# Kernel optimization log

Measured on AMD Instinct MI355X. Metric: run time of the kernel, lower is better.

## Reference

```python
import jax, jax.numpy as jnp
import numpy as np

NUM_HEADS = 16


def setup_inputs() -> dict:
    key = jax.random.key(0)
    ks = jax.random.split(key, 5)
    b, s, d = 2, 2048, 1024
    std = (2.0 / (d + d)) ** 0.5
    x = jax.random.normal(ks[0], (b, s, d), dtype=jnp.float32)
    Wq = jax.random.normal(ks[1], (d, d), dtype=jnp.float32) * std
    Wk = jax.random.normal(ks[2], (d, d), dtype=jnp.float32) * std
    Wv = jax.random.normal(ks[3], (d, d), dtype=jnp.float32) * std
    Wo = jax.random.normal(ks[4], (d, d), dtype=jnp.float32) * std
    return {"x": x, "Wq": Wq, "Wk": Wk, "Wv": Wv, "Wo": Wo}


def reference(x, Wq, Wk, Wv, Wo):
    b, s, d = x.shape
    h = NUM_HEADS
    dk = d // h
    # projections: bias-free x @ W (W is [in, out])
    def split_heads(t):
        return t.reshape(b, s, h, dk).transpose(0, 2, 1, 3)  # b h s dk
    q = split_heads(x @ Wq)
    k = split_heads(x @ Wk)
    v = split_heads(x @ Wv)
    scale = 1.0 / jnp.sqrt(jnp.asarray(dk, dtype=x.dtype))
    scores = jnp.einsum('bhqd,bhkd->bhqk', q, k) * scale  # b h s s
    causal = jnp.tril(jnp.ones((s, s), dtype=bool))
    scores = jnp.where(causal, scores, -jnp.inf)
    probs = jax.nn.softmax(scores, axis=-1)
    out = jnp.einsum('bhqk,bhkd->bhqd', probs, v)
    out = out.transpose(0, 2, 1, 3).reshape(b, s, d)  # b s (h dk)
    return out @ Wo
```

## Files before the change

kernel.cpp:

```cpp
#include <hip/hip_runtime.h>

typedef unsigned short u16;
typedef unsigned int   u32;

using bf16x8 = __attribute__((ext_vector_type(8))) __bf16;
using bf16x4 = __attribute__((ext_vector_type(4))) __bf16;
using f32x4  = __attribute__((ext_vector_type(4))) float;
using s16x4  = __attribute__((ext_vector_type(4))) short;

#define NH    16
#define DKH   64
#define SEQ   2048
#define BAT   2
#define DMOD  1024

#define QSCALE 0.18033688011112042f

__device__ __forceinline__ u16 f2bf(float f) {
  union { float f; u32 u; } v; v.f = f;
  u32 r = v.u + 0x7fffu + ((v.u >> 16) & 1u);
  return (u16)(r >> 16);
}

__device__ __forceinline__ u32 pack2bf(float a, float b) {
  union { float f; u32 u; } x, y; x.f = a; y.f = b;
  u32 ua = x.u + 0x7fffu + ((x.u >> 16) & 1u);
  u32 ub = y.u + 0x7fffu + ((y.u >> 16) & 1u);
  return __builtin_amdgcn_perm(ub, ua, 0x07060302u);
}

__device__ __forceinline__ s16x4 pk4bf(float a, float b, float c, float d) {
  union { bf16x4 bv; s16x4 sv; } u;
  u.bv[0] = (__bf16)a; u.bv[1] = (__bf16)b; u.bv[2] = (__bf16)c; u.bv[3] = (__bf16)d;
  return u.sv;
}

#if __has_builtin(__builtin_amdgcn_exp2f)
#define EXP2(x) __builtin_amdgcn_exp2f(x)
#else
#define EXP2(x) exp2f(x)
#endif

#if __has_builtin(__builtin_amdgcn_mfma_f32_16x16x16bf16_1k)
__device__ __forceinline__ f32x4 mfma16(s16x4 a, s16x4 b, f32x4 c) {
  return __builtin_amdgcn_mfma_f32_16x16x16bf16_1k(a, b, c, 0, 0, 0);
}
#else
__device__ __forceinline__ f32x4 mfma16(s16x4 a, s16x4 b, f32x4 c) {
  f32x4 d;
  asm volatile("v_mfma_f32_16x16x16_bf16 %0, %1, %2, %3\n\ts_nop 7\n\ts_nop 7"
               : "=v"(d) : "v"(a), "v"(b), "v"(c));
  return d;
}
#endif

typedef const __attribute__((address_space(1))) u32 glb_u32;
typedef __attribute__((address_space(3))) u32 lds_u32;
__device__ __forceinline__ void gload16(const u16* g, u16* l) {
  __builtin_amdgcn_global_load_lds((glb_u32*)(const void*)g, (lds_u32*)(void*)l, 16, 0, 0);
}

__global__ __launch_bounds__(256) void transpose_all(const float* __restrict__ Wq,
                                                     const float* __restrict__ Wk,
                                                     const float* __restrict__ Wv,
                                                     const float* __restrict__ Wo,
                                                     u16* __restrict__ Wt) {
  __shared__ u16 t[32][33];
  const float* W = blockIdx.z == 0 ? Wq : blockIdx.z == 1 ? Wk : blockIdx.z == 2 ? Wv : Wo;
  u16* o = Wt + (size_t)blockIdx.z * DMOD * DMOD;
  int bx = blockIdx.x * 32, by = blockIdx.y * 32;
  int x = threadIdx.x, y = threadIdx.y;
  #pragma unroll
  for (int i = 0; i < 32; i += 8)
    t[y + i][x] = f2bf(W[(size_t)(by + y + i) * DMOD + bx + x]);
  __syncthreads();
  #pragma unroll
  for (int i = 0; i < 32; i += 8)
    o[(size_t)(bx + y + i) * DMOD + by + x] = t[x][y + i];
}

__global__ __launch_bounds__(256) void convert_x(const float* __restrict__ x,
                                                 u16* __restrict__ xb) {
  size_t i = ((size_t)blockIdx.x * 256 + threadIdx.x) * 8;
  float4 f0 = *(const float4*)(x + i);
  float4 f1 = *(const float4*)(x + i + 4);
  uint4 o;
  o.x = pack2bf(f0.x, f0.y); o.y = pack2bf(f0.z, f0.w);
  o.z = pack2bf(f1.x, f1.y); o.w = pack2bf(f1.z, f1.w);
  *(uint4*)(xb + i) = o;
}

__global__ __launch_bounds__(256, 3) void gemm_qkv(const u16* __restrict__ A,
                                                   const u16* __restrict__ Bt,
                                                   u16* __restrict__ Qo,
                                                   u16* __restrict__ Ko,
                                                   u16* __restrict__ Vo) {
  __shared__ __align__(16) u16 As[128 * 32];
  __shared__ __align__(16) u16 Bs[128 * 32];
  const int tid  = threadIdx.x;
  const int lane = tid & 63, wv = tid >> 6;
  const int wm   = wv >> 1, wn = wv & 1;
  const int lrow = lane & 15, quad = lane >> 4;
  const int tileM = blockIdx.x * 128, tileN = blockIdx.y * 128;

  const f32x4 fz = {0.f, 0.f, 0.f, 0.f};
  f32x4 acc[4][4];
  #pragma unroll
  for (int i = 0; i < 4; ++i)
    #pragma unroll
    for (int j = 0; j < 4; ++j) acc[i][j] = fz;

  for (int kt = 0; kt < DMOD; kt += 32) {
    if (kt) __syncthreads();
    #pragma unroll
    for (int i = 0; i < 2; ++i) {
      int idx = i * 256 + tid;
      gload16(&A [(size_t)(tileM + (idx >> 2)) * DMOD + kt + (idx & 3) * 8], &As[idx * 8]);
      gload16(&Bt[(size_t)(tileN + (idx >> 2)) * DMOD + kt + (idx & 3) * 8], &Bs[idx * 8]);
    }
    __syncthreads();

    bf16x8 af[4], bfr[4];
    #pragma unroll
    for (int mt = 0; mt < 4; ++mt)
      af[mt] = *(const bf16x8*)(&As[(wm * 64 + mt * 16 + lrow) * 32 + quad * 8]);
    #pragma unroll
    for (int nt = 0; nt < 4; ++nt)
      bfr[nt] = *(const bf16x8*)(&Bs[(wn * 64 + nt * 16 + lrow) * 32 + quad * 8]);
    #pragma unroll
    for (int mt = 0; mt < 4; ++mt)
      #pragma unroll
      for (int nt = 0; nt < 4; ++nt)
        acc[mt][nt] = __builtin_amdgcn_mfma_f32_16x16x32_bf16(af[mt], bfr[nt],
                                                              acc[mt][nt], 0, 0, 0);
  }

  #pragma unroll
  for (int mt = 0; mt < 4; ++mt) {
    #pragma unroll
    for (int nt = 0; nt < 4; ++nt) {
      int gm0 = tileM + wm * 64 + mt * 16 + quad * 4;
      int gn  = tileN + wn * 64 + nt * 16 + lrow;
      int which = gn >> 10, col = gn & 1023;
      int bb = gm0 >> 11, srw0 = gm0 & (SEQ - 1);
      int hh = col >> 6, dki = col & (DKH - 1);
      size_t bhi = (size_t)(bb * NH + hh);
      if (which == 0) {
        #pragma unroll
        for (int r = 0; r < 4; ++r)
          Qo[(bhi * SEQ + srw0 + r) * DKH + dki] = f2bf(acc[mt][nt][r] * QSCALE);
      } else if (which == 1) {
        #pragma unroll
        for (int r = 0; r < 4; ++r)
          Ko[(bhi * SEQ + srw0 + r) * DKH + dki] = f2bf(acc[mt][nt][r]);
      } else {
        uint2 pk;
        pk.x = pack2bf(acc[mt][nt][0], acc[mt][nt][1]);
        pk.y = pack2bf(acc[mt][nt][2], acc[mt][nt][3]);
        *(uint2*)(&Vo[(((bhi * (SEQ / 4)) + (srw0 >> 2)) * DKH + dki) * 4]) = pk;
      }
    }
  }
}

__global__ __launch_bounds__(256, 3) void gemm_out(const u16* __restrict__ A,
                                                   const u16* __restrict__ Bt,
                                                   float* __restrict__ Co) {
  __shared__ __align__(16) u16 As[128 * 32];
  __shared__ __align__(16) u16 Bs[64 * 32];
  const int tid  = threadIdx.x;
  const int lane = tid & 63, wv = tid >> 6;
  const int wm   = wv & 1, wn = wv >> 1;
  const int lrow = lane & 15, quad = lane >> 4;
  const int tileM = blockIdx.x * 128, tileN = blockIdx.y * 64;

  const f32x4 fz = {0.f, 0.f, 0.f, 0.f};
  f32x4 acc[4][2];
  #pragma unroll
  for (int i = 0; i < 4; ++i) { acc[i][0] = fz; acc[i][1] = fz; }

  for (int kt = 0; kt < DMOD; kt += 32) {
    if (kt) __syncthreads();
    #pragma unroll
    for (int i = 0; i < 2; ++i) {
      int idx = i * 256 + tid;
      gload16(&A[(size_t)(tileM + (idx >> 2)) * DMOD + kt + (idx & 3) * 8], &As[idx * 8]);
    }
    gload16(&Bt[(size_t)(tileN + (tid >> 2)) * DMOD + kt + (tid & 3) * 8], &Bs[tid * 8]);
    __syncthreads();

    bf16x8 af[4], bfr[2];
    #pragma unroll
    for (int mt = 0; mt < 4; ++mt)
      af[mt] = *(const bf16x8*)(&As[(wm * 64 + mt * 16 + lrow) * 32 + quad * 8]);
    #pragma unroll
    for (int nt = 0; nt < 2; ++nt)
      bfr[nt] = *(const bf16x8*)(&Bs[(wn * 32 + nt * 16 + lrow) * 32 + quad * 8]);
    #pragma unroll
    for (int mt = 0; mt < 4; ++mt)
      #pragma unroll
      for (int nt = 0; nt < 2; ++nt)
        acc[mt][nt] = __builtin_amdgcn_mfma_f32_16x16x32_bf16(af[mt], bfr[nt],
                                                              acc[mt][nt], 0, 0, 0);
  }

  #pragma unroll
  for (int mt = 0; mt < 4; ++mt)
    #pragma unroll
    for (int nt = 0; nt < 2; ++nt)
      #pragma unroll
      for (int r = 0; r < 4; ++r) {
        int gm = tileM + wm * 64 + mt * 16 + quad * 4 + r;
        int gn = tileN + wn * 32 + nt * 16 + lrow;
        Co[(size_t)gm * DMOD + gn] = acc[mt][nt][r];
      }
}

#define KP 72
#define VP 132
#define OP 68

__global__ __launch_bounds__(256, 2) void attn_k(const u16* __restrict__ Q,
                                                 const u16* __restrict__ Kg,
                                                 const u16* __restrict__ Vg,
                                                 u16* __restrict__ Og) {
  __shared__ __align__(16) u16 KsA[128 * KP];
  __shared__ __align__(16) u16 VsA[64 * VP];
  __shared__ __align__(16) u16 KsB[128 * KP];
  __shared__ __align__(16) u16 VsB[64 * VP];

  const int tid  = threadIdx.x;
  const int lane = tid & 63, w = tid >> 6;
  const int lrow = lane & 15, quad = lane >> 4;
  const int bh = blockIdx.x;
  const int t  = blockIdx.y;
  const int qt = (t < 8) ? t : 23 - t;
  const int b = bh >> 4, h = bh & 15;

  const u16* Qbh = Q  + (size_t)bh * SEQ * DKH;
  const u16* Kbh = Kg + (size_t)bh * SEQ * DKH;
  const u16* Vbh = Vg + (size_t)bh * SEQ * DKH;

  const int jmax = qt;

  bf16x8 bq[2][2];
  #pragma unroll
  for (int s = 0; s < 2; ++s)
    #pragma unroll
    for (int kk = 0; kk < 2; ++kk)
      bq[s][kk] = *(const bf16x8*)(&Qbh[(size_t)(qt * 128 + (2 * w + s) * 16 + lrow) * DKH
                                        + kk * 32 + quad * 8]);

  uint4 kreg[4], vreg[4];
  #pragma unroll
  for (int k = 0; k < 4; ++k) {
    int ci = k * 256 + tid;
    kreg[k] = *(const uint4*)(&Kbh[(size_t)(ci >> 3) * DKH + (ci & 7) * 8]);
    vreg[k] = *(const uint4*)(&Vbh[(size_t)(ci >> 5) * 256 + (ci & 31) * 8]);
  }

  const f32x4 fz = {0.f, 0.f, 0.f, 0.f};
  f32x4 oacc[2][4];
  #pragma unroll
  for (int s = 0; s < 2; ++s)
    #pragma unroll
    for (int d = 0; d < 4; ++d) oacc[s][d] = fz;
  float lsum[2] = {0.f, 0.f};

  int cur = 0;
  for (int j = 0; j <= jmax; ++j) {
    u16* Ks = cur ? KsB : KsA;
    u16* Vs = cur ? VsB : VsA;

    #pragma unroll
    for (int k = 0; k < 4; ++k) {
      int ci = k * 256 + tid;
      *(uint4*)(&Ks[(ci >> 3) * KP + (ci & 7) * 8]) = kreg[k];
      int sq = ci >> 5, dkp = ci & 31;
      union { uint4 q; uint2 d[2]; } vv; vv.q = vreg[k];
      *(uint2*)(&Vs[(2 * dkp)     * VP + 4 * sq]) = vv.d[0];
      *(uint2*)(&Vs[(2 * dkp + 1) * VP + 4 * sq]) = vv.d[1];
    }

    if (j < jmax) {
      const int jn = j + 1;
      #pragma unroll
      for (int k = 0; k < 4; ++k) {
        int ci = k * 256 + tid;
        kreg[k] = *(const uint4*)(&Kbh[(size_t)(jn * 128 + (ci >> 3)) * DKH + (ci & 7) * 8]);
        vreg[k] = *(const uint4*)(&Vbh[(size_t)(jn * 32 + (ci >> 5)) * 256 + (ci & 31) * 8]);
      }
    }

    __syncthreads();

    if (j < jmax) {
      __builtin_amdgcn_s_setprio(1);
      f32x4 sacc[2][8];
      #pragma unroll
      for (int s = 0; s < 2; ++s)
        #pragma unroll
        for (int m = 0; m < 8; ++m) sacc[s][m] = fz;
      #pragma unroll
      for (int kk = 0; kk < 2; ++kk)
        #pragma unroll
        for (int m = 0; m < 8; ++m) {
          bf16x8 ak = *(const bf16x8*)(&Ks[(m * 16 + lrow) * KP + kk * 32 + quad * 8]);
          sacc[0][m] = __builtin_amdgcn_mfma_f32_16x16x32_bf16(ak, bq[0][kk], sacc[0][m], 0, 0, 0);
          sacc[1][m] = __builtin_amdgcn_mfma_f32_16x16x32_bf16(ak, bq[1][kk], sacc[1][m], 0, 0, 0);
        }
      #pragma unroll
      for (int m = 0; m < 8; ++m) {
        float p00 = EXP2(sacc[0][m][0]), p01 = EXP2(sacc[0][m][1]);
        float p02 = EXP2(sacc[0][m][2]), p03 = EXP2(sacc[0][m][3]);
        float p10 = EXP2(sacc[1][m][0]), p11 = EXP2(sacc[1][m][1]);
        float p12 = EXP2(sacc[1][m][2]), p13 = EXP2(sacc[1][m][3]);
        lsum[0] += (p00 + p01) + (p02 + p03);
        lsum[1] += (p10 + p11) + (p12 + p13);
        s16x4 pk0 = pk4bf(p00, p01, p02, p03);
        s16x4 pk1 = pk4bf(p10, p11, p12, p13);
        #pragma unroll
        for (int d = 0; d < 4; ++d) {
          s16x4 av = *(const s16x4*)(&Vs[(d * 16 + lrow) * VP + m * 16 + quad * 4]);
          oacc[0][d] = mfma16(av, pk0, oacc[0][d]);
          oacc[1][d] = mfma16(av, pk1, oacc[1][d]);
        }
      }
      __builtin_amdgcn_s_setprio(0);
    } else {
      #pragma unroll
      for (int s = 0; s < 2; ++s) {
        const int ss = 2 * w + s;
        for (int m = 0; m < ss; ++m) {
          f32x4 sv = fz;
          #pragma unroll
          for (int kk = 0; kk < 2; ++kk) {
            bf16x8 ak = *(const bf16x8*)(&Ks[(m * 16 + lrow) * KP + kk * 32 + quad * 8]);
            sv = __builtin_amdgcn_mfma_f32_16x16x32_bf16(ak, bq[s][kk], sv, 0, 0, 0);
          }
          float p0 = EXP2(sv[0]), p1 = EXP2(sv[1]), p2 = EXP2(sv[2]), p3 = EXP2(sv[3]);
          lsum[s] += (p0 + p1) + (p2 + p3);
          s16x4 pk = pk4bf(p0, p1, p2, p3);
          #pragma unroll
          for (int d = 0; d < 4; ++d) {
            s16x4 av = *(const s16x4*)(&Vs[(d * 16 + lrow) * VP + m * 16 + quad * 4]);
            oacc[s][d] = mfma16(av, pk, oacc[s][d]);
          }
        }
        {
          f32x4 sv = fz;
          #pragma unroll
          for (int kk = 0; kk < 2; ++kk) {
            bf16x8 ak = *(const bf16x8*)(&Ks[(ss * 16 + lrow) * KP + kk * 32 + quad * 8]);
            sv = __builtin_amdgcn_mfma_f32_16x16x32_bf16(ak, bq[s][kk], sv, 0, 0, 0);
          }
          float p[4];
          #pragma unroll
          for (int r = 0; r < 4; ++r)
            p[r] = (quad * 4 + r > lrow) ? 0.f : EXP2(sv[r]);
          lsum[s] += (p[0] + p[1]) + (p[2] + p[3]);
          s16x4 pk = pk4bf(p[0], p[1], p[2], p[3]);
          #pragma unroll
          for (int d = 0; d < 4; ++d) {
            s16x4 av = *(const s16x4*)(&Vs[(d * 16 + lrow) * VP + ss * 16 + quad * 4]);
            oacc[s][d] = mfma16(av, pk, oacc[s][d]);
          }
        }
      }
    }
    cur ^= 1;
  }

  float inv[2];
  #pragma unroll
  for (int s = 0; s < 2; ++s) {
    float v = lsum[s];
    v += __shfl_xor(v, 16, 64);
    v += __shfl_xor(v, 32, 64);
    inv[s] = 1.f / v;
  }

  __syncthreads();
  u16* Osr = KsA;
  #pragma unroll
  for (int s = 0; s < 2; ++s) {
    int row = (2 * w + s) * 16 + lrow;
    #pragma unroll
    for (int d = 0; d < 4; ++d) {
      uint2 pkk;
      pkk.x = pack2bf(oacc[s][d][0] * inv[s], oacc[s][d][1] * inv[s]);
      pkk.y = pack2bf(oacc[s][d][2] * inv[s], oacc[s][d][3] * inv[s]);
      *(uint2*)(&Osr[row * OP + d * 16 + quad * 4]) = pkk;
    }
  }
  __syncthreads();
  #pragma unroll
  for (int k = 0; k < 4; ++k) {
    int c = k * 256 + tid;
    int row = c >> 3, ch = c & 7;
    uint4 v = *(const uint4*)(&Osr[row * OP + ch * 8]);
    *(uint4*)(&Og[(size_t)(b * SEQ + qt * 128 + row) * DMOD + h * DKH + ch * 8]) = v;
  }
}

extern "C" void kernel_launch(void* const* d_in, const int* in_sizes, int n_in,
                              void* d_out, int out_size, void* d_ws, size_t ws_size,
                              hipStream_t stream) {
  const float* x  = (const float*)d_in[0];
  const float* Wq = (const float*)d_in[1];
  const float* Wk = (const float*)d_in[2];
  const float* Wv = (const float*)d_in[3];
  const float* Wo = (const float*)d_in[4];

  u16* ws = (u16*)d_ws;
  const size_t WSZ = (size_t)DMOD * DMOD;
  const size_t TSZ = (size_t)BAT * NH * SEQ * DKH;
  u16* Wt  = ws;
  u16* Wto = Wt + 3 * WSZ;
  u16* xb  = Wt + 4 * WSZ;
  u16* Qb  = xb + TSZ;
  u16* Kb  = Qb + TSZ;
  u16* Vb  = Kb + TSZ;
  u16* Ob  = xb;

  transpose_all<<<dim3(32, 32, 4), dim3(32, 8), 0, stream>>>(Wq, Wk, Wv, Wo, Wt);
  convert_x<<<dim3(2048), 256, 0, stream>>>(x, xb);

  gemm_qkv<<<dim3(32, 24), 256, 0, stream>>>(xb, Wt, Qb, Kb, Vb);

  attn_k<<<dim3(32, 16), 256, 0, stream>>>(Qb, Kb, Vb, Ob);

  gemm_out<<<dim3(32, 16), 256, 0, stream>>>(Ob, Wto, (float*)d_out);
}
```

Baseline: 181.1 us.

## Halve attention query tile, load K/V via direct-to-LDS swizzled loads

The attention kernel now uses 128-thread blocks, each owning 64 query rows, with twice as many blocks and a rotated block-to-query-tile mapping for causal load balance. K and V tiles are copied straight from global memory into LDS with gload16 using an XOR swizzle instead of register staging and padded LDS. V keeps its natural seq-major layout and is read with swizzled addressing. The register double buffering is dropped, so global loads no longer overlap compute and each iteration adds a barrier, in exchange for more blocks, better occupancy and fewer conflicted stores.

New measurement: 178.4 us. About the same (-1.5%).

```diff
diff --git a/kernel.cpp b/kernel.cpp
--- a/kernel.cpp
+++ b/kernel.cpp
@@ -216,48 +216,35 @@
       }
 }
 
-#define KP 72
-#define VP 132
 #define OP 68
 
-__global__ __launch_bounds__(256, 2) void attn_k(const u16* __restrict__ Q,
+__global__ __launch_bounds__(128, 2) void attn_k(const u16* __restrict__ Q,
                                                  const u16* __restrict__ Kg,
                                                  const u16* __restrict__ Vg,
                                                  u16* __restrict__ Og) {
-  __shared__ __align__(16) u16 KsA[128 * KP];
-  __shared__ __align__(16) u16 VsA[64 * VP];
-  __shared__ __align__(16) u16 KsB[128 * KP];
-  __shared__ __align__(16) u16 VsB[64 * VP];
+  __shared__ __align__(16) u16 Ks[128 * 64];
+  __shared__ __align__(16) u16 Vs[32 * 256];
 
   const int tid  = threadIdx.x;
   const int lane = tid & 63, w = tid >> 6;
   const int lrow = lane & 15, quad = lane >> 4;
   const int bh = blockIdx.x;
-  const int t  = blockIdx.y;
-  const int qt = (t < 8) ? t : 23 - t;
+  const int qb = (int)((blockIdx.y + bh) & 31);
   const int b = bh >> 4, h = bh & 15;
+  const int jmax = qb >> 1;
+  const int qoff = qb & 1;
 
   const u16* Qbh = Q  + (size_t)bh * SEQ * DKH;
   const u16* Kbh = Kg + (size_t)bh * SEQ * DKH;
   const u16* Vbh = Vg + (size_t)bh * SEQ * DKH;
 
-  const int jmax = qt;
-
   bf16x8 bq[2][2];
   #pragma unroll
   for (int s = 0; s < 2; ++s)
     #pragma unroll
     for (int kk = 0; kk < 2; ++kk)
-      bq[s][kk] = *(const bf16x8*)(&Qbh[(size_t)(qt * 128 + (2 * w + s) * 16 + lrow) * DKH
+      bq[s][kk] = *(const bf16x8*)(&Qbh[(size_t)(qb * 64 + (2 * w + s) * 16 + lrow) * DKH
                                         + kk * 32 + quad * 8]);
-
-  uint4 kreg[4], vreg[4];
-  #pragma unroll
-  for (int k = 0; k < 4; ++k) {
-    int ci = k * 256 + tid;
-    kreg[k] = *(const uint4*)(&Kbh[(size_t)(ci >> 3) * DKH + (ci & 7) * 8]);
-    vreg[k] = *(const uint4*)(&Vbh[(size_t)(ci >> 5) * 256 + (ci & 31) * 8]);
-  }
 
   const f32x4 fz = {0.f, 0.f, 0.f, 0.f};
   f32x4 oacc[2][4];
@@ -267,29 +254,20 @@
     for (int d = 0; d < 4; ++d) oacc[s][d] = fz;
   float lsum[2] = {0.f, 0.f};
 
-  int cur = 0;
   for (int j = 0; j <= jmax; ++j) {
-    u16* Ks = cur ? KsB : KsA;
-    u16* Vs = cur ? VsB : VsA;
-
-    #pragma unroll
-    for (int k = 0; k < 4; ++k) {
-      int ci = k * 256 + tid;
-      *(uint4*)(&Ks[(ci >> 3) * KP + (ci & 7) * 8]) = kreg[k];
-      int sq = ci >> 5, dkp = ci & 31;
-      union { uint4 q; uint2 d[2]; } vv; vv.q = vreg[k];
-      *(uint2*)(&Vs[(2 * dkp)     * VP + 4 * sq]) = vv.d[0];
-      *(uint2*)(&Vs[(2 * dkp + 1) * VP + 4 * sq]) = vv.d[1];
-    }
-
-    if (j < jmax) {
-      const int jn = j + 1;
-      #pragma unroll
-      for (int k = 0; k < 4; ++k) {
-        int ci = k * 256 + tid;
-        kreg[k] = *(const uint4*)(&Kbh[(size_t)(jn * 128 + (ci >> 3)) * DKH + (ci & 7) * 8]);
-        vreg[k] = *(const uint4*)(&Vbh[(size_t)(jn * 32 + (ci >> 5)) * 256 + (ci & 31) * 8]);
-      }
+    if (j) __syncthreads();
+
+    #pragma unroll
+    for (int i = 0; i < 8; ++i) {
+      int cD = i * 128 + tid;
+      int r = cD >> 3, c = cD & 7;
+      gload16(&Kbh[(size_t)(j * 128 + r) * DKH + ((c ^ (r & 7)) << 3)], &Ks[cD * 8]);
+    }
+    #pragma unroll
+    for (int i = 0; i < 8; ++i) {
+      int cD = i * 128 + tid;
+      int sq = cD >> 5, c = cD & 31;
+      gload16(&Vbh[(size_t)(j * 32 + sq) * 256 + ((c ^ (sq & 7)) << 3)], &Vs[cD * 8]);
     }
 
     __syncthreads();
@@ -305,7 +283,8 @@
       for (int kk = 0; kk < 2; ++kk)
         #pragma unroll
         for (int m = 0; m < 8; ++m) {
-          bf16x8 ak = *(const bf16x8*)(&Ks[(m * 16 + lrow) * KP + kk * 32 + quad * 8]);
+          bf16x8 ak = *(const bf16x8*)(&Ks[(m * 16 + lrow) * 64
+                                           + (((kk * 4 + quad) ^ (lrow & 7)) << 3)]);
           sacc[0][m] = __builtin_amdgcn_mfma_f32_16x16x32_bf16(ak, bq[0][kk], sacc[0][m], 0, 0, 0);
           sacc[1][m] = __builtin_amdgcn_mfma_f32_16x16x32_bf16(ak, bq[1][kk], sacc[1][m], 0, 0, 0);
         }
@@ -319,9 +298,12 @@
         lsum[1] += (p10 + p11) + (p12 + p13);
         s16x4 pk0 = pk4bf(p00, p01, p02, p03);
         s16x4 pk1 = pk4bf(p10, p11, p12, p13);
+        const int sq = m * 4 + quad;
         #pragma unroll
         for (int d = 0; d < 4; ++d) {
-          s16x4 av = *(const s16x4*)(&Vs[(d * 16 + lrow) * VP + m * 16 + quad * 4]);
+          int dk = d * 16 + lrow;
+          s16x4 av = *(const s16x4*)(&Vs[sq * 256
+                                         + ((((dk >> 1) ^ (sq & 7)) << 3) | ((dk & 1) << 2))]);
           oacc[0][d] = mfma16(av, pk0, oacc[0][d]);
           oacc[1][d] = mfma16(av, pk1, oacc[1][d]);
         }
@@ -330,20 +312,24 @@
     } else {
       #pragma unroll
       for (int s = 0; s < 2; ++s) {
-        const int ss = 2 * w + s;
-        for (int m = 0; m < ss; ++m) {
+        const int L = qoff * 4 + 2 * w + s;
+        for (int m = 0; m < L; ++m) {
           f32x4 sv = fz;
           #pragma unroll
           for (int kk = 0; kk < 2; ++kk) {
-            bf16x8 ak = *(const bf16x8*)(&Ks[(m * 16 + lrow) * KP + kk * 32 + quad * 8]);
+            bf16x8 ak = *(const bf16x8*)(&Ks[(m * 16 + lrow) * 64
+                                             + (((kk * 4 + quad) ^ (lrow & 7)) << 3)]);
             sv = __builtin_amdgcn_mfma_f32_16x16x32_bf16(ak, bq[s][kk], sv, 0, 0, 0);
           }
           float p0 = EXP2(sv[0]), p1 = EXP2(sv[1]), p2 = EXP2(sv[2]), p3 = EXP2(sv[3]);
           lsum[s] += (p0 + p1) + (p2 + p3);
           s16x4 pk = pk4bf(p0, p1, p2, p3);
+          const int sq = m * 4 + quad;
           #pragma unroll
           for (int d = 0; d < 4; ++d) {
-            s16x4 av = *(const s16x4*)(&Vs[(d * 16 + lrow) * VP + m * 16 + quad * 4]);
+            int dk = d * 16 + lrow;
+            s16x4 av = *(const s16x4*)(&Vs[sq * 256
+                                           + ((((dk >> 1) ^ (sq & 7)) << 3) | ((dk & 1) << 2))]);
             oacc[s][d] = mfma16(av, pk, oacc[s][d]);
           }
         }
@@ -351,7 +337,8 @@
           f32x4 sv = fz;
           #pragma unroll
           for (int kk = 0; kk < 2; ++kk) {
-            bf16x8 ak = *(const bf16x8*)(&Ks[(ss * 16 + lrow) * KP + kk * 32 + quad * 8]);
+            bf16x8 ak = *(const bf16x8*)(&Ks[(L * 16 + lrow) * 64
+                                             + (((kk * 4 + quad) ^ (lrow & 7)) << 3)]);
             sv = __builtin_amdgcn_mfma_f32_16x16x32_bf16(ak, bq[s][kk], sv, 0, 0, 0);
           }
           float p[4];
@@ -360,15 +347,17 @@
             p[r] = (quad * 4 + r > lrow) ? 0.f : EXP2(sv[r]);
           lsum[s] += (p[0] + p[1]) + (p[2] + p[3]);
           s16x4 pk = pk4bf(p[0], p[1], p[2], p[3]);
+          const int sq = L * 4 + quad;
           #pragma unroll
           for (int d = 0; d < 4; ++d) {
-            s16x4 av = *(const s16x4*)(&Vs[(d * 16 + lrow) * VP + ss * 16 + quad * 4]);
+            int dk = d * 16 + lrow;
+            s16x4 av = *(const s16x4*)(&Vs[sq * 256
+                                           + ((((dk >> 1) ^ (sq & 7)) << 3) | ((dk & 1) << 2))]);
             oacc[s][d] = mfma16(av, pk, oacc[s][d]);
           }
         }
       }
     }
-    cur ^= 1;
   }
 
   float inv[2];
@@ -381,7 +370,7 @@
   }
 
   __syncthreads();
-  u16* Osr = KsA;
+  u16* Osr = Ks;
   #pragma unroll
   for (int s = 0; s < 2; ++s) {
     int row = (2 * w + s) * 16 + lrow;
@@ -396,10 +385,10 @@
   __syncthreads();
   #pragma unroll
   for (int k = 0; k < 4; ++k) {
-    int c = k * 256 + tid;
+    int c = k * 128 + tid;
     int row = c >> 3, ch = c & 7;
     uint4 v = *(const uint4*)(&Osr[row * OP + ch * 8]);
-    *(uint4*)(&Og[(size_t)(b * SEQ + qt * 128 + row) * DMOD + h * DKH + ch * 8]) = v;
+    *(uint4*)(&Og[(size_t)(b * SEQ + qb * 64 + row) * DMOD + h * DKH + ch * 8]) = v;
   }
 }
 
@@ -428,7 +417,7 @@
 
   gemm_qkv<<<dim3(32, 24), 256, 0, stream>>>(xb, Wt, Qb, Kb, Vb);
 
-  attn_k<<<dim3(32, 16), 256, 0, stream>>>(Qb, Kb, Vb, Ob);
+  attn_k<<<dim3(32, 32), 128, 0, stream>>>(Qb, Kb, Vb, Ob);
 
   gemm_out<<<dim3(32, 16), 256, 0, stream>>>(Ob, Wto, (float*)d_out);
 }
```
